# Performance work log

Hardware: AMD Instinct MI355X
Metric: run time of the kernel (lower is better)

The kernel has to match this reference:

```python
import jax, jax.numpy as jnp
import numpy as np

N, S, D = 8, 1024, 512      # batch, seq_len, in_dim
H, KD, VD, OD = 8, 64, 64, 512  # heads, key_dim, value_dim, out_dim
GRAPH_WEIGHT = 0.5
NEG_INF = float('-inf')


def setup_inputs() -> dict:
    key = jax.random.key(0)
    ks = jax.random.split(key, 9)
    return {
        "x":    jax.random.normal(ks[0], (N, S, D), jnp.float32),
        "Wk":   jax.random.normal(ks[1], (H, D, KD), jnp.float32) * 0.02,
        "bk":   jax.random.normal(ks[2], (H, KD), jnp.float32) * 0.02,
        "Wv":   jax.random.normal(ks[3], (H, D, VD), jnp.float32) * 0.02,
        "bv":   jax.random.normal(ks[4], (H, VD), jnp.float32) * 0.02,
        "Wout": jax.random.normal(ks[5], (H * VD, OD), jnp.float32) * 0.02,
        "bout": jax.random.normal(ks[6], (OD,), jnp.float32) * 0.02,
        "graph": jax.random.normal(ks[7], (S, S), jnp.float32),
        "knn": 64,
    }


def reference(x, Wk, bk, Wv, bv, Wout, bout, graph, knn):
    # Per-head key/value projections (heads vectorized on leading axis h).
    k = jnp.einsum('nsd,hdk->hnsk', x, Wk) + bk[:, None, None, :]   # (H,N,S,KD)
    v = jnp.einsum('nsd,hdv->hnsv', x, Wv) + bv[:, None, None, :]   # (H,N,S,VD)
    q = k  # self-attention: query = key

    # att_unnorm = (q . k) / sqrt(key_dim)  -> (H,N,S,S)
    att = jnp.einsum('hnqk,hntk->hnqt', q, k) / np.sqrt(KD).astype(np.float32)

    # Causal mask (equivalent to the Python loop att[:, i, i+1:] = -inf).
    causal = jnp.tril(jnp.ones((S, S), dtype=bool))
    att = jnp.where(causal, att, NEG_INF)

    # knn top-k pooling: keep top-knn entries along the last axis, rest -> -inf.
    topv = jax.lax.top_k(att, knn)[0]                  # (H,N,S,knn)
    kth = topv[..., -1:]                               # kth largest per row
    att = jnp.where(att >= kth, att, NEG_INF)

    p = jax.nn.softmax(att, axis=-1)

    # Graph-weighted attention blend (graph is row-softmaxed at init time).
    att_graph = jax.nn.softmax(graph, axis=-1)         # (S,S)
    p = GRAPH_WEIGHT * att_graph + (1.0 - GRAPH_WEIGHT) * p

    # y_h = att @ value, then concat heads and output projection.
    y = jnp.einsum('hnqt,hntv->hnqv', p, v)            # (H,N,S,VD)
    y = y.transpose(1, 2, 0, 3).reshape(N, S, H * VD)  # head-major concat
    return y @ Wout + bout
```

## Files before the change

kernel.cpp:

```cpp
#include <hip/hip_runtime.h>
#include <math.h>

#define NB 8
#define SL 1024
#define DI 512
#define HH 8
#define KDN 64
#define VDN 64
#define ODN 512
#define ATT_SCALE 0.125f

#define KLO_OFF 2097152u
#define V_OFF   4194304u
#define G_OFF   8388608u
#define Y_OFF   9437184u

#define ORD_NEG_INF 0x007FFFFFu

typedef __attribute__((ext_vector_type(8))) short bf16x8;
typedef __attribute__((ext_vector_type(4))) float f32x4;

__device__ __forceinline__ unsigned fordu(float f) {
  unsigned b = __float_as_uint(f);
  return b ^ ((b & 0x80000000u) ? 0xFFFFFFFFu : 0x80000000u);
}
__device__ __forceinline__ float ifordu(unsigned k) {
  unsigned b = k ^ ((k & 0x80000000u) ? 0x80000000u : 0xFFFFFFFFu);
  return __uint_as_float(b);
}
__device__ __forceinline__ unsigned short f2bf(float f) {
  unsigned u = __float_as_uint(f);
  unsigned r = (u + 0x7FFFu + ((u >> 16) & 1u)) >> 16;
  return (unsigned short)r;
}
__device__ __forceinline__ float bf2f(unsigned short h) {
  return __uint_as_float(((unsigned)h) << 16);
}

__global__ __launch_bounds__(256) void kvproj_kernel(
    const float* __restrict__ x, const float* __restrict__ Wk, const float* __restrict__ bk,
    const float* __restrict__ Wv, const float* __restrict__ bv, float* __restrict__ ws)
{
  __shared__ float xs[64][68];
  __shared__ float wks[64][68];
  __shared__ float wvs[64][68];
  const int tid = threadIdx.x;
  const int tx = tid & 15, ty = tid >> 4;
  const int m0 = blockIdx.x * 64;
  const int h = blockIdx.y;
  const float* wkb = Wk + (size_t)h * (DI * KDN);
  const float* wvb = Wv + (size_t)h * (DI * VDN);
  float ak[4][4] = {{0.f}};
  float av[4][4] = {{0.f}};
  for (int dt = 0; dt < DI / 64; ++dt) {
    __syncthreads();
#pragma unroll
    for (int it = 0; it < 4; ++it) {
      const int r = ty + it * 16;
      const int c = tx * 4;
      *(float4*)&xs[r][c]  = *(const float4*)&x[(size_t)(m0 + r) * DI + dt * 64 + c];
      *(float4*)&wks[r][c] = *(const float4*)&wkb[(size_t)(dt * 64 + r) * KDN + c];
      *(float4*)&wvs[r][c] = *(const float4*)&wvb[(size_t)(dt * 64 + r) * VDN + c];
    }
    __syncthreads();
#pragma unroll 4
    for (int dd = 0; dd < 64; ++dd) {
      float a[4];
#pragma unroll
      for (int i = 0; i < 4; ++i) a[i] = xs[ty * 4 + i][dd];
      const float4 bkv = *(const float4*)&wks[dd][tx * 4];
      const float4 bvv = *(const float4*)&wvs[dd][tx * 4];
      const float bkj[4] = {bkv.x, bkv.y, bkv.z, bkv.w};
      const float bvj[4] = {bvv.x, bvv.y, bvv.z, bvv.w};
#pragma unroll
      for (int i = 0; i < 4; ++i) {
#pragma unroll
        for (int j = 0; j < 4; ++j) {
          ak[i][j] = __fmaf_rn(a[i], bkj[j], ak[i][j]);
          av[i][j] = __fmaf_rn(a[i], bvj[j], av[i][j]);
        }
      }
    }
  }
  const int n = m0 >> 10;
  const int s0 = m0 & 1023;
  float* vb = ws + V_OFF;
  unsigned short* khi = (unsigned short*)ws;
  unsigned short* klo = (unsigned short*)(ws + KLO_OFF);
#pragma unroll
  for (int i = 0; i < 4; ++i) {
    const int s = s0 + ty * 4 + i;
    float4 vv;
    vv.x = av[i][0] + bv[h * VDN + tx * 4 + 0];
    vv.y = av[i][1] + bv[h * VDN + tx * 4 + 1];
    vv.z = av[i][2] + bv[h * VDN + tx * 4 + 2];
    vv.w = av[i][3] + bv[h * VDN + tx * 4 + 3];
    *(float4*)&vb[((size_t)(h * NB + n) * SL + s) * VDN + tx * 4] = vv;
    union { unsigned short u[4]; uint2 v2; } ph, pl;
#pragma unroll
    for (int j = 0; j < 4; ++j) {
      const float kf = ak[i][j] + bk[h * KDN + tx * 4 + j];
      const unsigned short h16 = f2bf(kf);
      ph.u[j] = h16;
      pl.u[j] = f2bf(kf - bf2f(h16));
    }
    const size_t koff = ((size_t)(h * NB + n) * SL + s) * KDN + tx * 4;
    *(uint2*)&khi[koff] = ph.v2;
    *(uint2*)&klo[koff] = pl.v2;
  }
}

__global__ __launch_bounds__(256) void gsoftmax_kernel(const float* __restrict__ gin, float* __restrict__ ws)
{
  unsigned short* ghi = (unsigned short*)(ws + G_OFF);
  const int row = blockIdx.x;
  const int tid = threadIdx.x;
  const int lane = tid & 63, wave = tid >> 6;
  __shared__ float red[4];
  __shared__ float red2[4];
  float v[4];
  float m = -INFINITY;
#pragma unroll
  for (int i = 0; i < 4; ++i) {
    v[i] = gin[(size_t)row * SL + tid + i * 256];
    m = fmaxf(m, v[i]);
  }
#pragma unroll
  for (int off = 32; off; off >>= 1) m = fmaxf(m, __shfl_xor(m, off));
  if (lane == 0) red[wave] = m;
  __syncthreads();
  m = fmaxf(fmaxf(red[0], red[1]), fmaxf(red[2], red[3]));
  float e[4];
  float s = 0.f;
#pragma unroll
  for (int i = 0; i < 4; ++i) { e[i] = __expf(v[i] - m); s += e[i]; }
#pragma unroll
  for (int off = 32; off; off >>= 1) s += __shfl_xor(s, off);
  if (lane == 0) red2[wave] = s;
  __syncthreads();
  s = red2[0] + red2[1] + red2[2] + red2[3];
  const float inv = 1.0f / s;
#pragma unroll
  for (int i = 0; i < 4; ++i) ghi[(size_t)row * SL + tid + i * 256] = f2bf(e[i] * inv);
}

__global__ __launch_bounds__(512, 8) void attn_kernel(float* __restrict__ ws, const int* __restrict__ knn_p)
{
  __shared__ float S[16][260];
  const int tid = threadIdx.x;
  const int lane = tid & 63;
  const int wave = tid >> 6;
  const int q0 = blockIdx.x * 16;
  const int hn = blockIdx.y;
  const int h = hn >> 3, n = hn & 7;
  const int K = knn_p[0];
  const unsigned short* khi = (const unsigned short*)ws + (size_t)hn * SL * KDN;
  const unsigned short* klo = (const unsigned short*)(ws + KLO_OFF) + (size_t)hn * SL * KDN;
  const float* vb = ws + V_OFF + (size_t)hn * (SL * VDN);
  float* y = ws + Y_OFF;

  const int col = lane & 15, grp = lane >> 4;
  const bf16x8 a0h = *(const bf16x8*)&khi[(size_t)(q0 + col) * KDN + grp * 8];
  const bf16x8 a1h = *(const bf16x8*)&khi[(size_t)(q0 + col) * KDN + 32 + grp * 8];
  const bf16x8 a0l = *(const bf16x8*)&klo[(size_t)(q0 + col) * KDN + grp * 8];
  const bf16x8 a1l = *(const bf16x8*)&klo[(size_t)(q0 + col) * KDN + 32 + grp * 8];

  const int T = q0 / 16 + 1;
  const int rbase = wave * 2;

  float ev[2][8][2];
#pragma unroll
  for (int rr = 0; rr < 2; ++rr)
#pragma unroll
    for (int c = 0; c < 8; ++c) {
      ev[rr][c][0] = __uint_as_float(ORD_NEG_INF);
      ev[rr][c][1] = __uint_as_float(ORD_NEG_INF);
    }

#pragma unroll
  for (int ph = 0; ph < 4; ++ph) {
    const int tlo = ph * 16;
    const int thi = (T < tlo + 16) ? T : (tlo + 16);
    if (thi > tlo) {
      __syncthreads();
      for (int ti = tlo + wave; ti < thi; ti += 8) {
        const int t0 = ti * 16;
        const size_t bo = (size_t)(t0 + col) * KDN + grp * 8;
        const bf16x8 b0h = *(const bf16x8*)&khi[bo];
        const bf16x8 b1h = *(const bf16x8*)&khi[bo + 32];
        const bf16x8 b0l = *(const bf16x8*)&klo[bo];
        const bf16x8 b1l = *(const bf16x8*)&klo[bo + 32];
        f32x4 d = {0.f, 0.f, 0.f, 0.f};
        d = __builtin_amdgcn_mfma_f32_16x16x32_bf16(a0h, b0h, d, 0, 0, 0);
        d = __builtin_amdgcn_mfma_f32_16x16x32_bf16(a1h, b1h, d, 0, 0, 0);
        d = __builtin_amdgcn_mfma_f32_16x16x32_bf16(a0h, b0l, d, 0, 0, 0);
        d = __builtin_amdgcn_mfma_f32_16x16x32_bf16(a1h, b1l, d, 0, 0, 0);
        d = __builtin_amdgcn_mfma_f32_16x16x32_bf16(a0l, b0h, d, 0, 0, 0);
        d = __builtin_amdgcn_mfma_f32_16x16x32_bf16(a1l, b1h, d, 0, 0, 0);
        d = __builtin_amdgcn_mfma_f32_16x16x32_bf16(a0l, b0l, d, 0, 0, 0);
        d = __builtin_amdgcn_mfma_f32_16x16x32_bf16(a1l, b1l, d, 0, 0, 0);
        const int tl = t0 - ph * 256 + col;
#pragma unroll
        for (int r = 0; r < 4; ++r) S[grp * 4 + r][tl] = d[r];
      }
      __syncthreads();
#pragma unroll
      for (int rr = 0; rr < 2; ++rr) {
        const int q = q0 + rbase + rr;
        const int cmr = q >> 7;
#pragma unroll
        for (int cc = 0; cc < 2; ++cc) {
          const int c = ph * 2 + cc;
          if (c <= cmr) {
            const float2 sv = *(const float2*)&S[rbase + rr][cc * 128 + lane * 2];
            const int t0 = c * 128 + lane * 2;
            const unsigned k0 = (t0     <= q) ? fordu(sv.x * ATT_SCALE) : ORD_NEG_INF;
            const unsigned k1 = (t0 + 1 <= q) ? fordu(sv.y * ATT_SCALE) : ORD_NEG_INF;
            ev[rr][c][0] = __uint_as_float(k0);
            ev[rr][c][1] = __uint_as_float(k1);
          }
        }
      }
    }
  }
  __syncthreads();

  float* elist = (float*)((char*)&S[0][0] + wave * 768);
  unsigned short* tlist = (unsigned short*)(elist + 128);

#pragma unroll
  for (int rr = 0; rr < 2; ++rr) {
    const int q = q0 + rbase + rr;

    unsigned u[16];
#pragma unroll
    for (int c = 0; c < 8; ++c) {
      u[c * 2]     = __float_as_uint(ev[rr][c][0]);
      u[c * 2 + 1] = __float_as_uint(ev[rr][c][1]);
    }

    unsigned lmax = u[0];
#pragma unroll
    for (int i = 1; i < 16; ++i) lmax = lmax > u[i] ? lmax : u[i];
    unsigned mk = lmax, t0k = lmax;
#pragma unroll
    for (int off = 32; off; off >>= 1) {
      const unsigned om = (unsigned)__shfl_xor((int)mk, off);
      const unsigned ot = (unsigned)__shfl_xor((int)t0k, off);
      mk = mk > om ? mk : om;
      t0k = t0k < ot ? t0k : ot;
    }
    const float m = ifordu(mk);

    unsigned kth;
    if (q < K) {
      kth = ORD_NEG_INF;
    } else {
      unsigned lo = (K <= 64) ? t0k : 0u;
      unsigned hi = mk;
      while (lo < hi) {
        const unsigned mid = lo + ((hi - lo + 1) >> 1);
        int cnt = 0;
#pragma unroll
        for (int i = 0; i < 16; ++i)
          cnt += (int)__popcll(__ballot(u[i] >= mid));
        if (cnt >= K) lo = mid; else hi = mid - 1;
      }
      kth = lo;
    }

    float Z = 0.f;
#pragma unroll
    for (int c = 0; c < 8; ++c) {
#pragma unroll
      for (int j = 0; j < 2; ++j) {
        const unsigned k = u[c * 2 + j];
        float e = 0.f;
        if (k >= kth) e = __expf(ifordu(k) - m);
        ev[rr][c][j] = e;
        Z += e;
      }
    }
#pragma unroll
    for (int off = 32; off; off >>= 1) Z += __shfl_xor(Z, off);

    const unsigned long long lt = (1ull << lane) - 1ull;
    int cnt = 0;
#pragma unroll
    for (int c = 0; c < 8; ++c) {
#pragma unroll
      for (int j = 0; j < 2; ++j) {
        const float e = ev[rr][c][j];
        const unsigned long long msk = __ballot(e > 0.f);
        if (e > 0.f) {
          const int pos = cnt + (int)__popcll(msk & lt);
          if (pos < 128) {
            elist[pos] = e;
            tlist[pos] = (unsigned short)(c * 128 + lane * 2 + j);
          }
        }
        cnt += (int)__popcll(msk);
      }
    }
    cnt = (cnt < 128) ? cnt : 128;

    float yacc = 0.f;
    int i2 = 0;
    for (; i2 + 4 <= cnt; i2 += 4) {
      const float4 e4 = *(const float4*)&elist[i2];
      const ushort4 t4 = *(const ushort4*)&tlist[i2];
      yacc = __fmaf_rn(e4.x, vb[(size_t)t4.x * VDN + lane], yacc);
      yacc = __fmaf_rn(e4.y, vb[(size_t)t4.y * VDN + lane], yacc);
      yacc = __fmaf_rn(e4.z, vb[(size_t)t4.z * VDN + lane], yacc);
      yacc = __fmaf_rn(e4.w, vb[(size_t)t4.w * VDN + lane], yacc);
    }
    for (; i2 < cnt; ++i2) {
      yacc = __fmaf_rn(elist[i2], vb[(size_t)tlist[i2] * VDN + lane], yacc);
    }
    y[((size_t)(n * SL + q)) * ODN + h * VDN + lane] = yacc * (0.5f / Z);
  }
}

__global__ __launch_bounds__(256) void vtprep_kernel(float* __restrict__ ws)
{
  __shared__ float tile[64][65];
  const int t = threadIdx.x;
  const int t0 = blockIdx.x * 64;
  const int hn = blockIdx.y;
  const float* vb = ws + V_OFF + (size_t)hn * (SL * VDN);
  unsigned short* vthi = (unsigned short*)ws + (size_t)hn * VDN * SL;
  const int r = t >> 2, c4 = (t & 3) * 16;
#pragma unroll
  for (int j = 0; j < 4; ++j)
    *(float4*)&tile[r][c4 + j * 4] = *(const float4*)&vb[(size_t)(t0 + r) * VDN + c4 + j * 4];
  __syncthreads();
  union { unsigned short u[16]; uint4 v[2]; } hi;
#pragma unroll
  for (int j = 0; j < 16; ++j) hi.u[j] = f2bf(tile[c4 + j][r]);
  const size_t o = (size_t)r * SL + t0 + c4;
  *(uint4*)&vthi[o] = hi.v[0];
  *(uint4*)&vthi[o + 8] = hi.v[1];
}

__global__ __launch_bounds__(256) void gv_kernel(float* __restrict__ ws)
{
  const unsigned short* ghi = (const unsigned short*)(ws + G_OFF);
  const int tid = threadIdx.x;
  const int lane = tid & 63;
  const int wave = tid >> 6;
  const int col = lane & 15, grp = lane >> 4;
  const int q0 = blockIdx.x * 64;
  const int hn = blockIdx.y;
  const int h = hn >> 3, n = hn & 7;
  const unsigned short* vthi = (const unsigned short*)ws + (size_t)hn * VDN * SL;
  float* y = ws + Y_OFF;

  f32x4 acc[4];
#pragma unroll
  for (int odt = 0; odt < 4; ++odt) acc[odt] = (f32x4){0.f, 0.f, 0.f, 0.f};

  const size_t arow = (size_t)(q0 + wave * 16 + col) * SL;
  for (int ks = 0; ks < 32; ++ks) {
    const bf16x8 ah = *(const bf16x8*)&ghi[arow + ks * 32 + grp * 8];
#pragma unroll
    for (int odt = 0; odt < 4; ++odt) {
      const bf16x8 bh = *(const bf16x8*)&vthi[(size_t)(odt * 16 + col) * SL + ks * 32 + grp * 8];
      acc[odt] = __builtin_amdgcn_mfma_f32_16x16x32_bf16(ah, bh, acc[odt], 0, 0, 0);
    }
  }

#pragma unroll
  for (int odt = 0; odt < 4; ++odt) {
    const int vd = odt * 16 + col;
#pragma unroll
    for (int r = 0; r < 4; ++r) {
      const size_t off = ((size_t)(n * SL + q0 + wave * 16 + grp * 4 + r)) * ODN + h * VDN + vd;
      y[off] += 0.5f * acc[odt][r];
    }
  }
}

__global__ __launch_bounds__(256) void wtprep_kernel(const float* __restrict__ Wout, float* __restrict__ ws)
{
  __shared__ float tile[64][65];
  unsigned short* wth = (unsigned short*)(ws + KLO_OFF);
  unsigned short* wtl = wth + ODN * ODN;
  const int t = threadIdx.x;
  const int od0 = blockIdx.x * 64;
  const int k0 = blockIdx.y * 64;
  const int r = t >> 2, c4 = (t & 3) * 16;
#pragma unroll
  for (int j = 0; j < 4; ++j) {
    *(float4*)&tile[r][c4 + j * 4] = *(const float4*)&Wout[(size_t)(k0 + r) * ODN + od0 + c4 + j * 4];
  }
  __syncthreads();
  union { unsigned short u[16]; uint4 v[2]; } hi, lo;
#pragma unroll
  for (int j = 0; j < 16; ++j) {
    const float f = tile[c4 + j][r];
    const unsigned short h16 = f2bf(f);
    hi.u[j] = h16;
    lo.u[j] = f2bf(f - bf2f(h16));
  }
  const size_t o = (size_t)(od0 + r) * ODN + k0 + c4;
  *(uint4*)&wth[o] = hi.v[0];
  *(uint4*)&wth[o + 8] = hi.v[1];
  *(uint4*)&wtl[o] = lo.v[0];
  *(uint4*)&wtl[o + 8] = lo.v[1];
}

__global__ __launch_bounds__(256) void out_kernel(
    const float* __restrict__ bout, const float* __restrict__ ws, float* __restrict__ out)
{
  const unsigned short* wth = (const unsigned short*)(ws + KLO_OFF);
  const unsigned short* wtl = wth + ODN * ODN;
  const float* y = ws + Y_OFF;
  const int tid = threadIdx.x;
  const int lane = tid & 63;
  const int wave = tid >> 6;
  const int col = lane & 15, grp = lane >> 4;
  const int od0 = blockIdx.x * 64;
  const int m0 = blockIdx.y * 64 + wave * 16;

  f32x4 acc[4];
#pragma unroll
  for (int odt = 0; odt < 4; ++odt) acc[odt] = (f32x4){0.f, 0.f, 0.f, 0.f};

  const float* yrow = y + (size_t)(m0 + col) * ODN + grp * 8;
  for (int ks = 0; ks < 16; ++ks) {
    const float4 ya = *(const float4*)&yrow[ks * 32];
    const float4 yb = *(const float4*)&yrow[ks * 32 + 4];
    union { unsigned short u[8]; bf16x8 v; } ah, al;
    const float yf[8] = {ya.x, ya.y, ya.z, ya.w, yb.x, yb.y, yb.z, yb.w};
#pragma unroll
    for (int j = 0; j < 8; ++j) {
      const unsigned short h16 = f2bf(yf[j]);
      ah.u[j] = h16;
      al.u[j] = f2bf(yf[j] - bf2f(h16));
    }
#pragma unroll
    for (int odt = 0; odt < 4; ++odt) {
      const size_t bo = (size_t)(od0 + odt * 16 + col) * ODN + ks * 32 + grp * 8;
      const bf16x8 bh = *(const bf16x8*)&wth[bo];
      const bf16x8 bl = *(const bf16x8*)&wtl[bo];
      acc[odt] = __builtin_amdgcn_mfma_f32_16x16x32_bf16(ah.v, bh, acc[odt], 0, 0, 0);
      acc[odt] = __builtin_amdgcn_mfma_f32_16x16x32_bf16(ah.v, bl, acc[odt], 0, 0, 0);
      acc[odt] = __builtin_amdgcn_mfma_f32_16x16x32_bf16(al.v, bh, acc[odt], 0, 0, 0);
    }
  }

#pragma unroll
  for (int odt = 0; odt < 4; ++odt) {
    const int od = od0 + odt * 16 + col;
    const float bo = bout[od];
#pragma unroll
    for (int r = 0; r < 4; ++r) {
      out[(size_t)(m0 + grp * 4 + r) * ODN + od] = acc[odt][r] + bo;
    }
  }
}

extern "C" void kernel_launch(void* const* d_in, const int* in_sizes, int n_in,
                              void* d_out, int out_size, void* d_ws, size_t ws_size,
                              hipStream_t stream)
{
  const float* x     = (const float*)d_in[0];
  const float* Wk    = (const float*)d_in[1];
  const float* bk    = (const float*)d_in[2];
  const float* Wv    = (const float*)d_in[3];
  const float* bv    = (const float*)d_in[4];
  const float* Wout  = (const float*)d_in[5];
  const float* bout  = (const float*)d_in[6];
  const float* graph = (const float*)d_in[7];
  const int*   knn   = (const int*)d_in[8];
  float* out = (float*)d_out;
  float* ws  = (float*)d_ws;

  kvproj_kernel<<<dim3(128, 8), 256, 0, stream>>>(x, Wk, bk, Wv, bv, ws);
  gsoftmax_kernel<<<dim3(1024), 256, 0, stream>>>(graph, ws);
  attn_kernel<<<dim3(64, 64), 512, 0, stream>>>(ws, knn);
  vtprep_kernel<<<dim3(16, 64), 256, 0, stream>>>(ws);
  wtprep_kernel<<<dim3(8, 8), 256, 0, stream>>>(Wout, ws);
  gv_kernel<<<dim3(16, 64), 256, 0, stream>>>(ws);
  out_kernel<<<dim3(8, 128), 256, 0, stream>>>(bout, ws, out);
}
```

Measured before the change: 486.0 us.

## Give each wave one attention row and exponentiate only kept top-k entries

The attention kernel now launches 1024 threads per block, so each of the 16 waves owns one query row instead of two rows in sequence. This halves per-thread register state and doubles the waves available to hide latency. The softmax exponentials are now computed only for the compacted top-k survivors, up to two per lane, instead of for all 16 candidate scores per lane. The risk is that the larger block and the unchanged launch-bounds occupancy hint may cap registers and cause spills, or lower the number of blocks resident per CU.

Result: slower. 503.2 us (+3.5%).

```diff
diff --git a/kernel.cpp b/kernel.cpp
--- a/kernel.cpp
+++ b/kernel.cpp
@@ -144,7 +144,7 @@
   for (int i = 0; i < 4; ++i) ghi[(size_t)row * SL + tid + i * 256] = f2bf(e[i] * inv);
 }
 
-__global__ __launch_bounds__(512, 8) void attn_kernel(float* __restrict__ ws, const int* __restrict__ knn_p)
+__global__ __launch_bounds__(1024, 8) void attn_kernel(float* __restrict__ ws, const int* __restrict__ knn_p)
 {
   __shared__ float S[16][260];
   const int tid = threadIdx.x;
@@ -166,16 +166,14 @@
   const bf16x8 a1l = *(const bf16x8*)&klo[(size_t)(q0 + col) * KDN + 32 + grp * 8];
 
   const int T = q0 / 16 + 1;
-  const int rbase = wave * 2;
-
-  float ev[2][8][2];
-#pragma unroll
-  for (int rr = 0; rr < 2; ++rr)
-#pragma unroll
-    for (int c = 0; c < 8; ++c) {
-      ev[rr][c][0] = __uint_as_float(ORD_NEG_INF);
-      ev[rr][c][1] = __uint_as_float(ORD_NEG_INF);
-    }
+  const int q = q0 + wave;
+
+  float ev[8][2];
+#pragma unroll
+  for (int c = 0; c < 8; ++c) {
+    ev[c][0] = __uint_as_float(ORD_NEG_INF);
+    ev[c][1] = __uint_as_float(ORD_NEG_INF);
+  }
 
 #pragma unroll
   for (int ph = 0; ph < 4; ++ph) {
@@ -183,7 +181,7 @@
     const int thi = (T < tlo + 16) ? T : (tlo + 16);
     if (thi > tlo) {
       __syncthreads();
-      for (int ti = tlo + wave; ti < thi; ti += 8) {
+      for (int ti = tlo + wave; ti < thi; ti += 16) {
         const int t0 = ti * 16;
         const size_t bo = (size_t)(t0 + col) * KDN + grp * 8;
         const bf16x8 b0h = *(const bf16x8*)&khi[bo];
@@ -204,21 +202,17 @@
         for (int r = 0; r < 4; ++r) S[grp * 4 + r][tl] = d[r];
       }
       __syncthreads();
-#pragma unroll
-      for (int rr = 0; rr < 2; ++rr) {
-        const int q = q0 + rbase + rr;
-        const int cmr = q >> 7;
-#pragma unroll
-        for (int cc = 0; cc < 2; ++cc) {
-          const int c = ph * 2 + cc;
-          if (c <= cmr) {
-            const float2 sv = *(const float2*)&S[rbase + rr][cc * 128 + lane * 2];
-            const int t0 = c * 128 + lane * 2;
-            const unsigned k0 = (t0     <= q) ? fordu(sv.x * ATT_SCALE) : ORD_NEG_INF;
-            const unsigned k1 = (t0 + 1 <= q) ? fordu(sv.y * ATT_SCALE) : ORD_NEG_INF;
-            ev[rr][c][0] = __uint_as_float(k0);
-            ev[rr][c][1] = __uint_as_float(k1);
-          }
+      const int cmr = q >> 7;
+#pragma unroll
+      for (int cc = 0; cc < 2; ++cc) {
+        const int c = ph * 2 + cc;
+        if (c <= cmr) {
+          const float2 sv = *(const float2*)&S[wave][cc * 128 + lane * 2];
+          const int t0 = c * 128 + lane * 2;
+          const unsigned k0 = (t0     <= q) ? fordu(sv.x * ATT_SCALE) : ORD_NEG_INF;
+          const unsigned k1 = (t0 + 1 <= q) ? fordu(sv.y * ATT_SCALE) : ORD_NEG_INF;
+          ev[c][0] = __uint_as_float(k0);
+          ev[c][1] = __uint_as_float(k1);
         }
       }
     }
@@ -228,97 +222,93 @@
   float* elist = (float*)((char*)&S[0][0] + wave * 768);
   unsigned short* tlist = (unsigned short*)(elist + 128);
 
-#pragma unroll
-  for (int rr = 0; rr < 2; ++rr) {
-    const int q = q0 + rbase + rr;
-
-    unsigned u[16];
-#pragma unroll
-    for (int c = 0; c < 8; ++c) {
-      u[c * 2]     = __float_as_uint(ev[rr][c][0]);
-      u[c * 2 + 1] = __float_as_uint(ev[rr][c][1]);
-    }
-
-    unsigned lmax = u[0];
-#pragma unroll
-    for (int i = 1; i < 16; ++i) lmax = lmax > u[i] ? lmax : u[i];
-    unsigned mk = lmax, t0k = lmax;
-#pragma unroll
-    for (int off = 32; off; off >>= 1) {
-      const unsigned om = (unsigned)__shfl_xor((int)mk, off);
-      const unsigned ot = (unsigned)__shfl_xor((int)t0k, off);
-      mk = mk > om ? mk : om;
-      t0k = t0k < ot ? t0k : ot;
-    }
-    const float m = ifordu(mk);
-
-    unsigned kth;
-    if (q < K) {
-      kth = ORD_NEG_INF;
-    } else {
-      unsigned lo = (K <= 64) ? t0k : 0u;
-      unsigned hi = mk;
-      while (lo < hi) {
-        const unsigned mid = lo + ((hi - lo + 1) >> 1);
-        int cnt = 0;
-#pragma unroll
-        for (int i = 0; i < 16; ++i)
-          cnt += (int)__popcll(__ballot(u[i] >= mid));
-        if (cnt >= K) lo = mid; else hi = mid - 1;
+  unsigned lmax = __float_as_uint(ev[0][0]);
+#pragma unroll
+  for (int c = 0; c < 8; ++c) {
+    const unsigned a = __float_as_uint(ev[c][0]);
+    const unsigned b = __float_as_uint(ev[c][1]);
+    lmax = lmax > a ? lmax : a;
+    lmax = lmax > b ? lmax : b;
+  }
+  unsigned mk = lmax, t0k = lmax;
+#pragma unroll
+  for (int off = 32; off; off >>= 1) {
+    const unsigned om = (unsigned)__shfl_xor((int)mk, off);
+    const unsigned ot = (unsigned)__shfl_xor((int)t0k, off);
+    mk = mk > om ? mk : om;
+    t0k = t0k < ot ? t0k : ot;
+  }
+  const float m = ifordu(mk);
+
+  unsigned kth;
+  if (q < K) {
+    kth = ORD_NEG_INF;
+  } else {
+    unsigned lo = (K <= 64) ? t0k : 0u;
+    unsigned hi = mk;
+    while (lo < hi) {
+      const unsigned mid = lo + ((hi - lo + 1) >> 1);
+      int cnt = 0;
+#pragma unroll
+      for (int c = 0; c < 8; ++c) {
+        cnt += (int)__popcll(__ballot(__float_as_uint(ev[c][0]) >= mid));
+        cnt += (int)__popcll(__ballot(__float_as_uint(ev[c][1]) >= mid));
       }
-      kth = lo;
-    }
-
-    float Z = 0.f;
-#pragma unroll
-    for (int c = 0; c < 8; ++c) {
-#pragma unroll
-      for (int j = 0; j < 2; ++j) {
-        const unsigned k = u[c * 2 + j];
-        float e = 0.f;
-        if (k >= kth) e = __expf(ifordu(k) - m);
-        ev[rr][c][j] = e;
-        Z += e;
+      if (cnt >= K) lo = mid; else hi = mid - 1;
+    }
+    kth = lo;
+  }
+
+  const unsigned long long lt = (1ull << lane) - 1ull;
+  int cnt = 0;
+#pragma unroll
+  for (int c = 0; c < 8; ++c) {
+#pragma unroll
+    for (int j = 0; j < 2; ++j) {
+      const unsigned k = __float_as_uint(ev[c][j]);
+      const bool keep = (k >= kth) && (k != ORD_NEG_INF);
+      const unsigned long long msk = __ballot(keep);
+      if (keep) {
+        const int pos = cnt + (int)__popcll(msk & lt);
+        if (pos < 128) {
+          elist[pos] = ev[c][j];
+          tlist[pos] = (unsigned short)(c * 128 + lane * 2 + j);
+        }
       }
-    }
-#pragma unroll
-    for (int off = 32; off; off >>= 1) Z += __shfl_xor(Z, off);
-
-    const unsigned long long lt = (1ull << lane) - 1ull;
-    int cnt = 0;
-#pragma unroll
-    for (int c = 0; c < 8; ++c) {
-#pragma unroll
-      for (int j = 0; j < 2; ++j) {
-        const float e = ev[rr][c][j];
-        const unsigned long long msk = __ballot(e > 0.f);
-        if (e > 0.f) {
-          const int pos = cnt + (int)__popcll(msk & lt);
-          if (pos < 128) {
-            elist[pos] = e;
-            tlist[pos] = (unsigned short)(c * 128 + lane * 2 + j);
-          }
-        }
-        cnt += (int)__popcll(msk);
-      }
-    }
-    cnt = (cnt < 128) ? cnt : 128;
-
-    float yacc = 0.f;
-    int i2 = 0;
-    for (; i2 + 4 <= cnt; i2 += 4) {
-      const float4 e4 = *(const float4*)&elist[i2];
-      const ushort4 t4 = *(const ushort4*)&tlist[i2];
-      yacc = __fmaf_rn(e4.x, vb[(size_t)t4.x * VDN + lane], yacc);
-      yacc = __fmaf_rn(e4.y, vb[(size_t)t4.y * VDN + lane], yacc);
-      yacc = __fmaf_rn(e4.z, vb[(size_t)t4.z * VDN + lane], yacc);
-      yacc = __fmaf_rn(e4.w, vb[(size_t)t4.w * VDN + lane], yacc);
-    }
-    for (; i2 < cnt; ++i2) {
-      yacc = __fmaf_rn(elist[i2], vb[(size_t)tlist[i2] * VDN + lane], yacc);
-    }
-    y[((size_t)(n * SL + q)) * ODN + h * VDN + lane] = yacc * (0.5f / Z);
-  }
+      cnt += (int)__popcll(msk);
+    }
+  }
+  cnt = (cnt < 128) ? cnt : 128;
+
+  float zp = 0.f;
+  if (lane < cnt) {
+    const float e = __expf(ifordu(__float_as_uint(elist[lane])) - m);
+    elist[lane] = e;
+    zp += e;
+  }
+  if (lane + 64 < cnt) {
+    const float e = __expf(ifordu(__float_as_uint(elist[lane + 64])) - m);
+    elist[lane + 64] = e;
+    zp += e;
+  }
+  float Z = zp;
+#pragma unroll
+  for (int off = 32; off; off >>= 1) Z += __shfl_xor(Z, off);
+
+  float yacc = 0.f;
+  int i2 = 0;
+  for (; i2 + 4 <= cnt; i2 += 4) {
+    const float4 e4 = *(const float4*)&elist[i2];
+    const ushort4 t4 = *(const ushort4*)&tlist[i2];
+    yacc = __fmaf_rn(e4.x, vb[(size_t)t4.x * VDN + lane], yacc);
+    yacc = __fmaf_rn(e4.y, vb[(size_t)t4.y * VDN + lane], yacc);
+    yacc = __fmaf_rn(e4.z, vb[(size_t)t4.z * VDN + lane], yacc);
+    yacc = __fmaf_rn(e4.w, vb[(size_t)t4.w * VDN + lane], yacc);
+  }
+  for (; i2 < cnt; ++i2) {
+    yacc = __fmaf_rn(elist[i2], vb[(size_t)tlist[i2] * VDN + lane], yacc);
+  }
+  y[((size_t)(n * SL + q)) * ODN + h * VDN + lane] = yacc * (0.5f / Z);
 }
 
 __global__ __launch_bounds__(256) void vtprep_kernel(float* __restrict__ ws)
@@ -478,7 +468,7 @@
 
   kvproj_kernel<<<dim3(128, 8), 256, 0, stream>>>(x, Wk, bk, Wv, bv, ws);
   gsoftmax_kernel<<<dim3(1024), 256, 0, stream>>>(graph, ws);
-  attn_kernel<<<dim3(64, 64), 512, 0, stream>>>(ws, knn);
+  attn_kernel<<<dim3(64, 64), 1024, 0, stream>>>(ws, knn);
   vtprep_kernel<<<dim3(16, 64), 256, 0, stream>>>(ws);
   wtprep_kernel<<<dim3(8, 8), 256, 0, stream>>>(Wout, ws);
   gv_kernel<<<dim3(16, 64), 256, 0, stream>>>(ws);
```

## Fuse V transpose into projection kernel and store V as bf16

Applied to the files above, without the earlier changes.

The kv projection kernel now writes V directly as bf16 and also writes a transposed bf16 copy through shared memory, so the separate vtprep kernel launch and its fp32 V round-trip are removed. The attention gather reads bf16 V and converts it to float, halving the bytes of its scattered loads. Storing V in bf16 lowers the precision of the sparse attention-times-V product. Two extra block barriers and reuse of the xs tile are added to the projection kernel.

Result: no change. 486.9 us (+0.2%).

```diff
diff --git a/kernel.cpp b/kernel.cpp
--- a/kernel.cpp
+++ b/kernel.cpp
@@ -84,29 +84,41 @@
   }
   const int n = m0 >> 10;
   const int s0 = m0 & 1023;
-  float* vb = ws + V_OFF;
+  unsigned short* vbf = (unsigned short*)(ws + V_OFF);
+  unsigned short* vtb = vbf + 4194304u;
   unsigned short* khi = (unsigned short*)ws;
   unsigned short* klo = (unsigned short*)(ws + KLO_OFF);
+  const size_t hnbase = (size_t)(h * NB + n) * SL;
+  __syncthreads();
 #pragma unroll
   for (int i = 0; i < 4; ++i) {
     const int s = s0 + ty * 4 + i;
-    float4 vv;
-    vv.x = av[i][0] + bv[h * VDN + tx * 4 + 0];
-    vv.y = av[i][1] + bv[h * VDN + tx * 4 + 1];
-    vv.z = av[i][2] + bv[h * VDN + tx * 4 + 2];
-    vv.w = av[i][3] + bv[h * VDN + tx * 4 + 3];
-    *(float4*)&vb[((size_t)(h * NB + n) * SL + s) * VDN + tx * 4] = vv;
-    union { unsigned short u[4]; uint2 v2; } ph, pl;
+    union { unsigned short u[4]; uint2 v2; } pv_, ph, pl;
 #pragma unroll
     for (int j = 0; j < 4; ++j) {
+      const float vf = av[i][j] + bv[h * VDN + tx * 4 + j];
+      xs[ty * 4 + i][tx * 4 + j] = vf;
+      pv_.u[j] = f2bf(vf);
       const float kf = ak[i][j] + bk[h * KDN + tx * 4 + j];
       const unsigned short h16 = f2bf(kf);
       ph.u[j] = h16;
       pl.u[j] = f2bf(kf - bf2f(h16));
     }
-    const size_t koff = ((size_t)(h * NB + n) * SL + s) * KDN + tx * 4;
+    *(uint2*)&vbf[(hnbase + s) * VDN + tx * 4] = pv_.v2;
+    const size_t koff = (hnbase + s) * KDN + tx * 4;
     *(uint2*)&khi[koff] = ph.v2;
     *(uint2*)&klo[koff] = pl.v2;
+  }
+  __syncthreads();
+  {
+    const int r = tid >> 2, c4 = (tid & 3) * 16;
+    union { unsigned short u[16]; uint4 v[2]; } hi;
+#pragma unroll
+    for (int j = 0; j < 16; ++j) hi.u[j] = f2bf(xs[c4 + j][r]);
+    unsigned short* vt = vtb + hnbase * VDN;
+    const size_t o = (size_t)r * SL + s0 + c4;
+    *(uint4*)&vt[o] = hi.v[0];
+    *(uint4*)&vt[o + 8] = hi.v[1];
   }
 }
 
@@ -156,7 +168,7 @@
   const int K = knn_p[0];
   const unsigned short* khi = (const unsigned short*)ws + (size_t)hn * SL * KDN;
   const unsigned short* klo = (const unsigned short*)(ws + KLO_OFF) + (size_t)hn * SL * KDN;
-  const float* vb = ws + V_OFF + (size_t)hn * (SL * VDN);
+  const unsigned short* vb = (const unsigned short*)(ws + V_OFF) + (size_t)hn * (SL * VDN);
   float* y = ws + Y_OFF;
 
   const int col = lane & 15, grp = lane >> 4;
@@ -309,37 +321,20 @@
     for (; i2 + 4 <= cnt; i2 += 4) {
       const float4 e4 = *(const float4*)&elist[i2];
       const ushort4 t4 = *(const ushort4*)&tlist[i2];
-      yacc = __fmaf_rn(e4.x, vb[(size_t)t4.x * VDN + lane], yacc);
-      yacc = __fmaf_rn(e4.y, vb[(size_t)t4.y * VDN + lane], yacc);
-      yacc = __fmaf_rn(e4.z, vb[(size_t)t4.z * VDN + lane], yacc);
-      yacc = __fmaf_rn(e4.w, vb[(size_t)t4.w * VDN + lane], yacc);
+      const float v0 = bf2f(vb[(size_t)t4.x * VDN + lane]);
+      const float v1 = bf2f(vb[(size_t)t4.y * VDN + lane]);
+      const float v2 = bf2f(vb[(size_t)t4.z * VDN + lane]);
+      const float v3 = bf2f(vb[(size_t)t4.w * VDN + lane]);
+      yacc = __fmaf_rn(e4.x, v0, yacc);
+      yacc = __fmaf_rn(e4.y, v1, yacc);
+      yacc = __fmaf_rn(e4.z, v2, yacc);
+      yacc = __fmaf_rn(e4.w, v3, yacc);
     }
     for (; i2 < cnt; ++i2) {
-      yacc = __fmaf_rn(elist[i2], vb[(size_t)tlist[i2] * VDN + lane], yacc);
+      yacc = __fmaf_rn(elist[i2], bf2f(vb[(size_t)tlist[i2] * VDN + lane]), yacc);
     }
     y[((size_t)(n * SL + q)) * ODN + h * VDN + lane] = yacc * (0.5f / Z);
   }
-}
-
-__global__ __launch_bounds__(256) void vtprep_kernel(float* __restrict__ ws)
-{
-  __shared__ float tile[64][65];
-  const int t = threadIdx.x;
-  const int t0 = blockIdx.x * 64;
-  const int hn = blockIdx.y;
-  const float* vb = ws + V_OFF + (size_t)hn * (SL * VDN);
-  unsigned short* vthi = (unsigned short*)ws + (size_t)hn * VDN * SL;
-  const int r = t >> 2, c4 = (t & 3) * 16;
-#pragma unroll
-  for (int j = 0; j < 4; ++j)
-    *(float4*)&tile[r][c4 + j * 4] = *(const float4*)&vb[(size_t)(t0 + r) * VDN + c4 + j * 4];
-  __syncthreads();
-  union { unsigned short u[16]; uint4 v[2]; } hi;
-#pragma unroll
-  for (int j = 0; j < 16; ++j) hi.u[j] = f2bf(tile[c4 + j][r]);
-  const size_t o = (size_t)r * SL + t0 + c4;
-  *(uint4*)&vthi[o] = hi.v[0];
-  *(uint4*)&vthi[o + 8] = hi.v[1];
 }
 
 __global__ __launch_bounds__(256) void gv_kernel(float* __restrict__ ws)
@@ -352,7 +347,7 @@
   const int q0 = blockIdx.x * 64;
   const int hn = blockIdx.y;
   const int h = hn >> 3, n = hn & 7;
-  const unsigned short* vthi = (const unsigned short*)ws + (size_t)hn * VDN * SL;
+  const unsigned short* vthi = (const unsigned short*)(ws + V_OFF) + 4194304u + (size_t)hn * VDN * SL;
   float* y = ws + Y_OFF;
 
   f32x4 acc[4];
@@ -479,7 +474,6 @@
   kvproj_kernel<<<dim3(128, 8), 256, 0, stream>>>(x, Wk, bk, Wv, bv, ws);
   gsoftmax_kernel<<<dim3(1024), 256, 0, stream>>>(graph, ws);
   attn_kernel<<<dim3(64, 64), 512, 0, stream>>>(ws, knn);
-  vtprep_kernel<<<dim3(16, 64), 256, 0, stream>>>(ws);
   wtprep_kernel<<<dim3(8, 8), 256, 0, stream>>>(Wout, ws);
   gv_kernel<<<dim3(16, 64), 256, 0, stream>>>(ws);
   out_kernel<<<dim3(8, 128), 256, 0, stream>>>(bout, ws, out);
```
